# Kernel tuning notes

Measured on AMD Instinct MI355X. Metric: run time of the kernel, lower is better.

Reference implementation:

```python
import jax, jax.numpy as jnp
import numpy as np

B, T, EMB_D, HEAD = 8, 2048, 1024, 128


def setup_inputs() -> dict:
    key = jax.random.key(0)
    ks = jax.random.split(key, 7)
    s = 1.0 / np.sqrt(EMB_D)
    return {
        "inputs": jax.random.normal(ks[0], (B, T, EMB_D), dtype=jnp.float32),
        "Wk": jax.random.uniform(ks[1], (EMB_D, HEAD), jnp.float32, -s, s),
        "bk": jax.random.uniform(ks[2], (HEAD,), jnp.float32, -s, s),
        "Wq": jax.random.uniform(ks[3], (EMB_D, HEAD), jnp.float32, -s, s),
        "bq": jax.random.uniform(ks[4], (HEAD,), jnp.float32, -s, s),
        "Wv": jax.random.uniform(ks[5], (EMB_D, HEAD), jnp.float32, -s, s),
        "bv": jax.random.uniform(ks[6], (HEAD,), jnp.float32, -s, s),
    }


def reference(inputs, Wk, bk, Wq, bq, Wv, bv):
    # inputs: [B, T, C]
    Bq, Tq, _ = inputs.shape
    k = inputs @ Wk + bk  # [B, T, H]
    q = inputs @ Wq + bq
    v = inputs @ Wv + bv
    scale = HEAD ** -0.5
    weights = jnp.einsum("bth,bsh->bts", q, k) * scale  # [B, T, T]
    causal = jnp.tril(jnp.ones((Tq, Tq), dtype=bool))
    weights = jnp.where(causal, weights, -jnp.inf)
    # NOTE: original code applies softmax over dim=1 (the query axis), faithfully reproduced
    weights = jax.nn.softmax(weights, axis=1)
    return jnp.einsum("bts,bsh->bth", weights, v)  # [B, T, H]
```

## Files before the change

### kernel.cpp

```cpp
#include <hip/hip_runtime.h>
#include <hip/hip_bf16.h>

#define T_SEQ 2048
#define NBATCH 8
#define EMB 1024
#define HD 128

typedef _Float16 f16_t;
typedef _Float16 f16x8 __attribute__((ext_vector_type(8)));
typedef _Float16 f16x4 __attribute__((ext_vector_type(4)));
typedef float f32x4 __attribute__((ext_vector_type(4)));


__device__ __forceinline__ void g2l(const f16_t* g, f16_t* l) {
    __builtin_amdgcn_global_load_lds(
        (const __attribute__((address_space(1))) unsigned int*)g,
        (__attribute__((address_space(3))) unsigned int*)l, 16, 0, 0);
}

__global__ __launch_bounds__(256) void prep(
    const float* __restrict__ Wk, const float* __restrict__ bk,
    const float* __restrict__ Wq, const float* __restrict__ bq,
    const float* __restrict__ Wv, const float* __restrict__ bv,
    f16_t* __restrict__ w2, float* __restrict__ biasc,
    float4* __restrict__ out4, float4* __restrict__ colsum4) {
    int bid = blockIdx.x;
    int t = threadIdx.x;
    if (bid < 384) {
        int n = bid;
        const float scale = 0.08838834764831845f;
        const float* W; const float* bias; float sc; int col;
        if (n < 128)      { W = Wq; bias = bq; sc = scale; col = n; }
        else if (n < 256) { W = Wk; bias = bk; sc = 1.0f;  col = n - 128; }
        else              { W = Wv; bias = bv; sc = 1.0f;  col = n - 256; }
        if (t < 128) {
            int k0 = t * 8;
            f16x8 v;
            #pragma unroll
            for (int i = 0; i < 8; ++i) v[i] = (f16_t)(W[(size_t)(k0 + i) * HD + col] * sc);
            *(f16x8*)&w2[(size_t)(n >> 4) * 16384 + (size_t)(k0 >> 3) * 128 + (n & 15) * 8] = v;
        }
        if (t == 0) biasc[n] = bias[col] * sc;
    } else if (bid < 384 + 2048) {
        out4[(size_t)(bid - 384) * 256 + t] = make_float4(0.f, 0.f, 0.f, 0.f);
    } else {
        colsum4[(size_t)(bid - 2432) * 256 + t] = make_float4(0.f, 0.f, 0.f, 0.f);
    }
}

__global__ __launch_bounds__(256) void qkv_gemm(
    const float* __restrict__ X, const f16_t* __restrict__ w2,
    const float* __restrict__ biasc,
    f16_t* __restrict__ q2, f16_t* __restrict__ k2, f16_t* __restrict__ v2) {
    __shared__ f16_t Xs[2][64 * 72];
    __shared__ __align__(16) f16_t Bl[2][8 * 1024];

    int bid = blockIdx.x;
    int r8 = bid & 7, g = bid >> 3;
    int band = (g / 3) * 8 + r8;
    int i = g % 3;
    int m0 = band * 64, n0 = i * 128;
    int tid = threadIdx.x;
    int lane = tid & 63, w = tid >> 6;
    int quad = lane >> 4, l15 = lane & 15;
    int msub = (w & 1) * 32, nsub = (w >> 1) * 64;

    int srow = tid >> 2;
    int scg  = (tid & 3) * 16;

    const float* xrow = X + (size_t)(m0 + srow) * EMB + scg;
    const f16_t* bbase = w2 + (size_t)(n0 >> 4) * 16384;

    f32x4 acc[2][4] = {};
    float4 pf[4];

    auto loadA = [&](int kc) {
        #pragma unroll
        for (int u = 0; u < 4; ++u) pf[u] = *(const float4*)(xrow + kc * 64 + u * 4);
    };
    auto stageB = [&](int kc, int buf) {
        const f16_t* bsrc = bbase + (size_t)kc * 1024;
        #pragma unroll
        for (int ii = 0; ii < 4; ++ii) {
            int D = tid * 16 + ii * 4096;
            g2l(bsrc + (size_t)(D >> 11) * 16384 + ((D & 2047) >> 1),
                &Bl[buf][D >> 1]);
        }
    };
    auto stageA = [&](int buf) {
        union { f16_t h[8]; uint4 u4; } p0, p1;
        p0.h[0] = (f16_t)pf[0].x; p0.h[1] = (f16_t)pf[0].y;
        p0.h[2] = (f16_t)pf[0].z; p0.h[3] = (f16_t)pf[0].w;
        p0.h[4] = (f16_t)pf[1].x; p0.h[5] = (f16_t)pf[1].y;
        p0.h[6] = (f16_t)pf[1].z; p0.h[7] = (f16_t)pf[1].w;
        p1.h[0] = (f16_t)pf[2].x; p1.h[1] = (f16_t)pf[2].y;
        p1.h[2] = (f16_t)pf[2].z; p1.h[3] = (f16_t)pf[2].w;
        p1.h[4] = (f16_t)pf[3].x; p1.h[5] = (f16_t)pf[3].y;
        p1.h[6] = (f16_t)pf[3].z; p1.h[7] = (f16_t)pf[3].w;
        *(uint4*)&Xs[buf][srow * 72 + scg] = p0.u4;
        *(uint4*)&Xs[buf][srow * 72 + scg + 8] = p1.u4;
    };
    auto compute = [&](int buf) {
        #pragma unroll
        for (int ks = 0; ks < 2; ++ks) {
            f16x8 afr0 = *(const f16x8*)&Xs[buf][(msub + l15) * 72 + ks * 32 + quad * 8];
            f16x8 afr1 = *(const f16x8*)&Xs[buf][(msub + 16 + l15) * 72 + ks * 32 + quad * 8];
            #pragma unroll
            for (int nf = 0; nf < 4; ++nf) {
                int ntl = (nsub >> 4) + nf;
                f16x8 bfr = *(const f16x8*)&Bl[buf][ntl * 1024 + (ks * 4 + quad) * 128 + l15 * 8];
                acc[0][nf] = __builtin_amdgcn_mfma_f32_16x16x32_f16(afr0, bfr, acc[0][nf], 0, 0, 0);
                acc[1][nf] = __builtin_amdgcn_mfma_f32_16x16x32_f16(afr1, bfr, acc[1][nf], 0, 0, 0);
            }
        }
    };

    loadA(0);
    stageB(0, 0);
    stageA(0);
    __syncthreads();

    for (int kc = 0; kc < 16; ++kc) {
        int cur = kc & 1, nxt = cur ^ 1;
        if (kc + 1 < 16) {
            loadA(kc + 1);
            stageB(kc + 1, nxt);
        }
        compute(cur);
        if (kc + 1 < 16) stageA(nxt);
        __syncthreads();
    }

    #pragma unroll
    for (int nf = 0; nf < 4; ++nf) {
        int ng = n0 + nsub + nf * 16 + l15;
        float bval = biasc[ng];
        #pragma unroll
        for (int mf = 0; mf < 2; ++mf) {
            int rowg = m0 + msub + mf * 16 + quad * 4;
            f32x4 a = acc[mf][nf];
            if (ng < 256) {
                f16_t* dst = (ng < 128) ? q2 : k2;
                int c = ng & 127;
                #pragma unroll
                for (int r = 0; r < 4; ++r) {
                    int row = rowg + r;
                    dst[(size_t)(row >> 4) * 2048 + (c >> 3) * 128 + (row & 15) * 8 + (c & 7)]
                        = (f16_t)(a[r] + bval);
                }
            } else {
                int h = ng - 256;
                f16x4 hv;
                #pragma unroll
                for (int r = 0; r < 4; ++r) hv[r] = (f16_t)(a[r] + bval);
                *(f16x4*)&v2[(size_t)(rowg >> 3) * 1024 + h * 8 + (rowg & 7)] = hv;
            }
        }
    }
}

__global__ __launch_bounds__(256, 4) void col_stats(
    const f16_t* __restrict__ q2, const f16_t* __restrict__ k2,
    float* __restrict__ colsum) {
    __shared__ __align__(16) f16_t Ql[4 * 2048];

    int bid = blockIdx.x;
    int b = bid & 7;
    int item = 143 - (bid >> 3);
    int cg = 0, slab = 0, cum = 0;
    for (int c = 0; c < 32; ++c) {
        int n = (32 - c + 3) >> 2;
        if (item < cum + n) { cg = c; slab = item - cum; break; }
        cum += n;
    }
    int tc0 = cg + slab * 4, tc1 = min(tc0 + 4, 32);

    int tid = threadIdx.x, lane = tid & 63, w = tid >> 6;
    int quad = lane >> 4, l15 = lane & 15;
    int brow = b * 128;
    size_t base = (size_t)b * T_SEQ;

    f16x8 bfrs[4][4];
    #pragma unroll
    for (int st = 0; st < 4; ++st) {
        const f16_t* kt = k2 + (size_t)(brow + cg * 4 + st) * 2048 + l15 * 8;
        #pragma unroll
        for (int kf = 0; kf < 4; ++kf)
            bfrs[st][kf] = *(const f16x8*)(kt + (kf * 4 + quad) * 128);
    }

    float lacc[4] = {0.f, 0.f, 0.f, 0.f};

    for (int tc = tc0; tc < tc1; ++tc) {
        int tb = tc * 64;
        __syncthreads();
        const f16_t* qsrc = q2 + (size_t)(brow + tc * 4) * 2048;
        #pragma unroll
        for (int i = 0; i < 4; ++i)
            g2l(qsrc + i * 2048 + tid * 8, Ql + i * 2048 + tid * 8);
        __syncthreads();

        f16x8 afr[4];
        #pragma unroll
        for (int kf = 0; kf < 4; ++kf)
            afr[kf] = *(const f16x8*)&Ql[w * 2048 + (kf * 4 + quad) * 128 + l15 * 8];
        #pragma unroll
        for (int st = 0; st < 4; ++st) {
            f32x4 s = {};
            #pragma unroll
            for (int kf = 0; kf < 4; ++kf)
                s = __builtin_amdgcn_mfma_f32_16x16x32_f16(afr[kf], bfrs[st][kf], s, 0, 0, 0);
            int scol = cg * 64 + st * 16 + l15;
            #pragma unroll
            for (int r = 0; r < 4; ++r) {
                int t = tb + w * 16 + quad * 4 + r;
                if (t >= scol) lacc[st] += __expf(s[r]);
            }
        }
    }

    #pragma unroll
    for (int st = 0; st < 4; ++st) {
        float v = lacc[st];
        v += __shfl_xor(v, 16, 64);
        v += __shfl_xor(v, 32, 64);
        if (quad == 0) atomicAdd(&colsum[base + cg * 64 + st * 16 + l15], v);
    }
}

__global__ __launch_bounds__(256, 4) void attn_out(
    const f16_t* __restrict__ q2, const f16_t* __restrict__ k2,
    const f16_t* __restrict__ v2, const float* __restrict__ colsum,
    float* __restrict__ out) {
    __shared__ __align__(16) f16_t Kl[4 * 2048];
    __shared__ __align__(16) f16_t Vl[8 * 1024];
    __shared__ __align__(16) f16_t Pl[32 * 72];

    int bid = blockIdx.x;
    int b = bid & 7;
    int item = 159 - (bid >> 3);
    int g = 0, slab = 0, cum = 0;
    for (int gg = 0; gg < 64; ++gg) {
        int n = (((gg >> 1) + 1) + 7) >> 3;
        if (item < cum + n) { g = gg; slab = item - cum; break; }
        cum += n;
    }
    int nch = (g >> 1) + 1;
    int c0 = slab * 8, c1 = min(c0 + 8, nch);
    int trow = g * 32;

    int tid = threadIdx.x, lane = tid & 63, w = tid >> 6;
    int quad = lane >> 4, l15 = lane & 15;
    int brow = b * 128;
    size_t base = (size_t)b * T_SEQ;

    f16x8 qfr[2][4];
    #pragma unroll
    for (int tt = 0; tt < 2; ++tt) {
        const f16_t* qt = q2 + (size_t)(brow + 2 * g + tt) * 2048 + l15 * 8;
        #pragma unroll
        for (int kf = 0; kf < 4; ++kf)
            qfr[tt][kf] = *(const f16x8*)(qt + (kf * 4 + quad) * 128);
    }

    f32x4 o[2][2] = {};

    for (int c = c0; c < c1; ++c) {
        int sb = c * 64;
        __syncthreads();
        const f16_t* ksrc = k2 + (size_t)(brow + (sb >> 4)) * 2048;
        const f16_t* vsrc = v2 + (((size_t)base + sb) >> 3) * 1024;
        #pragma unroll
        for (int i = 0; i < 4; ++i) {
            g2l(ksrc + i * 2048 + tid * 8, Kl + i * 2048 + tid * 8);
            g2l(vsrc + i * 2048 + tid * 8, Vl + i * 2048 + tid * 8);
        }
        __syncthreads();

        float iv = 1.0f / colsum[base + sb + w * 16 + l15];
        int scol = sb + w * 16 + l15;
        f16x8 bfr[4];
        #pragma unroll
        for (int kf = 0; kf < 4; ++kf)
            bfr[kf] = *(const f16x8*)&Kl[w * 2048 + (kf * 4 + quad) * 128 + l15 * 8];
        #pragma unroll
        for (int tt = 0; tt < 2; ++tt) {
            f32x4 s = {};
            #pragma unroll
            for (int kf = 0; kf < 4; ++kf)
                s = __builtin_amdgcn_mfma_f32_16x16x32_f16(qfr[tt][kf], bfr[kf], s, 0, 0, 0);
            #pragma unroll
            for (int r = 0; r < 4; ++r) {
                int t = trow + tt * 16 + quad * 4 + r;
                float pv = (t >= scol) ? __expf(s[r]) * iv : 0.f;
                Pl[(tt * 16 + quad * 4 + r) * 72 + w * 16 + l15] = (f16_t)pv;
            }
        }
        __syncthreads();

        #pragma unroll
        for (int kf2 = 0; kf2 < 2; ++kf2) {
            f16x8 pa0 = *(const f16x8*)&Pl[(l15) * 72 + kf2 * 32 + quad * 8];
            f16x8 pa1 = *(const f16x8*)&Pl[(16 + l15) * 72 + kf2 * 32 + quad * 8];
            #pragma unroll
            for (int hh = 0; hh < 2; ++hh) {
                f16x8 vfr = *(const f16x8*)&Vl[(kf2 * 4 + quad) * 1024 + (w * 32 + hh * 16 + l15) * 8];
                o[0][hh] = __builtin_amdgcn_mfma_f32_16x16x32_f16(pa0, vfr, o[0][hh], 0, 0, 0);
                o[1][hh] = __builtin_amdgcn_mfma_f32_16x16x32_f16(pa1, vfr, o[1][hh], 0, 0, 0);
            }
        }
    }

    #pragma unroll
    for (int tt = 0; tt < 2; ++tt)
        #pragma unroll
        for (int hh = 0; hh < 2; ++hh)
            #pragma unroll
            for (int r = 0; r < 4; ++r)
                atomicAdd(&out[(base + trow + tt * 16 + quad * 4 + r) * HD + w * 32 + hh * 16 + l15],
                          o[tt][hh][r]);
}

extern "C" void kernel_launch(void* const* d_in, const int* in_sizes, int n_in,
                              void* d_out, int out_size, void* d_ws, size_t ws_size,
                              hipStream_t stream) {
    const float* X  = (const float*)d_in[0];
    const float* Wk = (const float*)d_in[1];
    const float* bk = (const float*)d_in[2];
    const float* Wq = (const float*)d_in[3];
    const float* bq = (const float*)d_in[4];
    const float* Wv = (const float*)d_in[5];
    const float* bv = (const float*)d_in[6];
    float* out = (float*)d_out;

    char* ws = (char*)d_ws;
    const size_t W2_B    = 24 * 16384 * 2;
    const size_t BIAS_B  = 2048;
    const size_t QKV_B   = (size_t)NBATCH * T_SEQ * HD * 2;
    f16_t* w2     = (f16_t*)ws;
    float* biasc  = (float*)(ws + W2_B);
    f16_t* q2     = (f16_t*)(ws + W2_B + BIAS_B);
    f16_t* k2     = (f16_t*)(ws + W2_B + BIAS_B + QKV_B);
    f16_t* v2     = (f16_t*)(ws + W2_B + BIAS_B + 2 * QKV_B);
    float* colsum = (float*)(ws + W2_B + BIAS_B + 3 * QKV_B);

    prep<<<dim3(2448), dim3(256), 0, stream>>>(Wk, bk, Wq, bq, Wv, bv, w2, biasc,
                                               (float4*)out, (float4*)colsum);
    qkv_gemm<<<dim3(768), dim3(256), 0, stream>>>(X, w2, biasc, q2, k2, v2);
    col_stats<<<dim3(1152), dim3(256), 0, stream>>>(q2, k2, colsum);
    attn_out<<<dim3(1280), dim3(256), 0, stream>>>(q2, k2, v2, colsum, out);
}
```

Measured before the change: 174.4 us.

## Load MFMA operands directly from global memory instead of staging through LDS

Across three kernels, operands that were staged in shared memory are now loaded straight from global memory into registers in MFMA fragment layout. In the QKV GEMM the X tile is converted to fp16 in registers rather than written to LDS. In col_stats the Q chunk is loaded per wave. In attn_out the K and V chunks are loaded per wave, with one barrier kept per iteration to guard the P buffer and occupancy lowered to 3 blocks. This removes LDS traffic and barriers but makes more strided global loads rely on L2/L1, and adds register pressure.

```diff
diff --git a/kernel.cpp b/kernel.cpp
--- a/kernel.cpp
+++ b/kernel.cpp
@@ -52,7 +52,6 @@
     const float* __restrict__ X, const f16_t* __restrict__ w2,
     const float* __restrict__ biasc,
     f16_t* __restrict__ q2, f16_t* __restrict__ k2, f16_t* __restrict__ v2) {
-    __shared__ f16_t Xs[2][64 * 72];
     __shared__ __align__(16) f16_t Bl[2][8 * 1024];
 
     int bid = blockIdx.x;
@@ -65,18 +64,33 @@
     int quad = lane >> 4, l15 = lane & 15;
     int msub = (w & 1) * 32, nsub = (w >> 1) * 64;
 
-    int srow = tid >> 2;
-    int scg  = (tid & 3) * 16;
-
-    const float* xrow = X + (size_t)(m0 + srow) * EMB + scg;
+    const float* abase = X + (size_t)(m0 + msub + l15) * EMB + quad * 8;
     const f16_t* bbase = w2 + (size_t)(n0 >> 4) * 16384;
 
     f32x4 acc[2][4] = {};
-    float4 pf[4];
-
-    auto loadA = [&](int kc) {
-        #pragma unroll
-        for (int u = 0; u < 4; ++u) pf[u] = *(const float4*)(xrow + kc * 64 + u * 4);
+    float4 araw[4][2];
+    f16x8 af[4];
+
+    auto loadAraw = [&](int kc) {
+        #pragma unroll
+        for (int mf = 0; mf < 2; ++mf)
+            #pragma unroll
+            for (int ks = 0; ks < 2; ++ks) {
+                const float* p = abase + (size_t)mf * (16 * EMB) + kc * 64 + ks * 32;
+                araw[mf * 2 + ks][0] = *(const float4*)p;
+                araw[mf * 2 + ks][1] = *(const float4*)(p + 4);
+            }
+    };
+    auto cvtA = [&]() {
+        #pragma unroll
+        for (int q = 0; q < 4; ++q) {
+            f16x8 v;
+            v[0] = (f16_t)araw[q][0].x; v[1] = (f16_t)araw[q][0].y;
+            v[2] = (f16_t)araw[q][0].z; v[3] = (f16_t)araw[q][0].w;
+            v[4] = (f16_t)araw[q][1].x; v[5] = (f16_t)araw[q][1].y;
+            v[6] = (f16_t)araw[q][1].z; v[7] = (f16_t)araw[q][1].w;
+            af[q] = v;
+        }
     };
     auto stageB = [&](int kc, int buf) {
         const f16_t* bsrc = bbase + (size_t)kc * 1024;
@@ -87,47 +101,31 @@
                 &Bl[buf][D >> 1]);
         }
     };
-    auto stageA = [&](int buf) {
-        union { f16_t h[8]; uint4 u4; } p0, p1;
-        p0.h[0] = (f16_t)pf[0].x; p0.h[1] = (f16_t)pf[0].y;
-        p0.h[2] = (f16_t)pf[0].z; p0.h[3] = (f16_t)pf[0].w;
-        p0.h[4] = (f16_t)pf[1].x; p0.h[5] = (f16_t)pf[1].y;
-        p0.h[6] = (f16_t)pf[1].z; p0.h[7] = (f16_t)pf[1].w;
-        p1.h[0] = (f16_t)pf[2].x; p1.h[1] = (f16_t)pf[2].y;
-        p1.h[2] = (f16_t)pf[2].z; p1.h[3] = (f16_t)pf[2].w;
-        p1.h[4] = (f16_t)pf[3].x; p1.h[5] = (f16_t)pf[3].y;
-        p1.h[6] = (f16_t)pf[3].z; p1.h[7] = (f16_t)pf[3].w;
-        *(uint4*)&Xs[buf][srow * 72 + scg] = p0.u4;
-        *(uint4*)&Xs[buf][srow * 72 + scg + 8] = p1.u4;
-    };
     auto compute = [&](int buf) {
         #pragma unroll
-        for (int ks = 0; ks < 2; ++ks) {
-            f16x8 afr0 = *(const f16x8*)&Xs[buf][(msub + l15) * 72 + ks * 32 + quad * 8];
-            f16x8 afr1 = *(const f16x8*)&Xs[buf][(msub + 16 + l15) * 72 + ks * 32 + quad * 8];
+        for (int ks = 0; ks < 2; ++ks)
             #pragma unroll
             for (int nf = 0; nf < 4; ++nf) {
                 int ntl = (nsub >> 4) + nf;
                 f16x8 bfr = *(const f16x8*)&Bl[buf][ntl * 1024 + (ks * 4 + quad) * 128 + l15 * 8];
-                acc[0][nf] = __builtin_amdgcn_mfma_f32_16x16x32_f16(afr0, bfr, acc[0][nf], 0, 0, 0);
-                acc[1][nf] = __builtin_amdgcn_mfma_f32_16x16x32_f16(afr1, bfr, acc[1][nf], 0, 0, 0);
-            }
-        }
+                acc[0][nf] = __builtin_amdgcn_mfma_f32_16x16x32_f16(af[ks], bfr, acc[0][nf], 0, 0, 0);
+                acc[1][nf] = __builtin_amdgcn_mfma_f32_16x16x32_f16(af[2 + ks], bfr, acc[1][nf], 0, 0, 0);
+            }
     };
 
-    loadA(0);
+    loadAraw(0);
     stageB(0, 0);
-    stageA(0);
+    cvtA();
     __syncthreads();
 
     for (int kc = 0; kc < 16; ++kc) {
-        int cur = kc & 1, nxt = cur ^ 1;
+        int cur = kc & 1;
         if (kc + 1 < 16) {
-            loadA(kc + 1);
-            stageB(kc + 1, nxt);
+            loadAraw(kc + 1);
+            stageB(kc + 1, cur ^ 1);
         }
         compute(cur);
-        if (kc + 1 < 16) stageA(nxt);
+        if (kc + 1 < 16) cvtA();
         __syncthreads();
     }
 
@@ -162,8 +160,6 @@
 __global__ __launch_bounds__(256, 4) void col_stats(
     const f16_t* __restrict__ q2, const f16_t* __restrict__ k2,
     float* __restrict__ colsum) {
-    __shared__ __align__(16) f16_t Ql[4 * 2048];
-
     int bid = blockIdx.x;
     int b = bid & 7;
     int item = 143 - (bid >> 3);
@@ -193,17 +189,11 @@
 
     for (int tc = tc0; tc < tc1; ++tc) {
         int tb = tc * 64;
-        __syncthreads();
-        const f16_t* qsrc = q2 + (size_t)(brow + tc * 4) * 2048;
-        #pragma unroll
-        for (int i = 0; i < 4; ++i)
-            g2l(qsrc + i * 2048 + tid * 8, Ql + i * 2048 + tid * 8);
-        __syncthreads();
-
         f16x8 afr[4];
+        const f16_t* qt = q2 + (size_t)(brow + tc * 4 + w) * 2048 + l15 * 8;
         #pragma unroll
         for (int kf = 0; kf < 4; ++kf)
-            afr[kf] = *(const f16x8*)&Ql[w * 2048 + (kf * 4 + quad) * 128 + l15 * 8];
+            afr[kf] = *(const f16x8*)(qt + (kf * 4 + quad) * 128);
         #pragma unroll
         for (int st = 0; st < 4; ++st) {
             f32x4 s = {};
@@ -228,12 +218,10 @@
     }
 }
 
-__global__ __launch_bounds__(256, 4) void attn_out(
+__global__ __launch_bounds__(256, 3) void attn_out(
     const f16_t* __restrict__ q2, const f16_t* __restrict__ k2,
     const f16_t* __restrict__ v2, const float* __restrict__ colsum,
     float* __restrict__ out) {
-    __shared__ __align__(16) f16_t Kl[4 * 2048];
-    __shared__ __align__(16) f16_t Vl[8 * 1024];
     __shared__ __align__(16) f16_t Pl[32 * 72];
 
     int bid = blockIdx.x;
@@ -267,22 +255,21 @@
 
     for (int c = c0; c < c1; ++c) {
         int sb = c * 64;
-        __syncthreads();
-        const f16_t* ksrc = k2 + (size_t)(brow + (sb >> 4)) * 2048;
-        const f16_t* vsrc = v2 + (((size_t)base + sb) >> 3) * 1024;
-        #pragma unroll
-        for (int i = 0; i < 4; ++i) {
-            g2l(ksrc + i * 2048 + tid * 8, Kl + i * 2048 + tid * 8);
-            g2l(vsrc + i * 2048 + tid * 8, Vl + i * 2048 + tid * 8);
-        }
-        __syncthreads();
-
+        f16x8 bfr[4];
+        const f16_t* kt = k2 + (size_t)(brow + (sb >> 4) + w) * 2048 + l15 * 8;
+        #pragma unroll
+        for (int kf = 0; kf < 4; ++kf)
+            bfr[kf] = *(const f16x8*)(kt + (kf * 4 + quad) * 128);
+        f16x8 vfr[2][2];
+        const f16_t* vt = v2 + ((size_t)(base + sb) >> 3) * 1024;
+        #pragma unroll
+        for (int kf2 = 0; kf2 < 2; ++kf2)
+            #pragma unroll
+            for (int hh = 0; hh < 2; ++hh)
+                vfr[kf2][hh] = *(const f16x8*)&vt[(kf2 * 4 + quad) * 1024 +
+                                                  (w * 32 + hh * 16 + l15) * 8];
         float iv = 1.0f / colsum[base + sb + w * 16 + l15];
         int scol = sb + w * 16 + l15;
-        f16x8 bfr[4];
-        #pragma unroll
-        for (int kf = 0; kf < 4; ++kf)
-            bfr[kf] = *(const f16x8*)&Kl[w * 2048 + (kf * 4 + quad) * 128 + l15 * 8];
         #pragma unroll
         for (int tt = 0; tt < 2; ++tt) {
             f32x4 s = {};
@@ -304,11 +291,11 @@
             f16x8 pa1 = *(const f16x8*)&Pl[(16 + l15) * 72 + kf2 * 32 + quad * 8];
             #pragma unroll
             for (int hh = 0; hh < 2; ++hh) {
-                f16x8 vfr = *(const f16x8*)&Vl[(kf2 * 4 + quad) * 1024 + (w * 32 + hh * 16 + l15) * 8];
-                o[0][hh] = __builtin_amdgcn_mfma_f32_16x16x32_f16(pa0, vfr, o[0][hh], 0, 0, 0);
-                o[1][hh] = __builtin_amdgcn_mfma_f32_16x16x32_f16(pa1, vfr, o[1][hh], 0, 0, 0);
-            }
-        }
+                o[0][hh] = __builtin_amdgcn_mfma_f32_16x16x32_f16(pa0, vfr[kf2][hh], o[0][hh], 0, 0, 0);
+                o[1][hh] = __builtin_amdgcn_mfma_f32_16x16x32_f16(pa1, vfr[kf2][hh], o[1][hh], 0, 0, 0);
+            }
+        }
+        __syncthreads();
     }
 
     #pragma unroll
```

Result: slower. 192.2 us (+10.2%).

## Drop LDS staging; split key chunks across waves with register-resident P

Applied to the files above, without the earlier changes.

col_stats now reads Q fragments straight from global memory instead of staging them through LDS, which removes two barriers per tile. attn_out is restructured so each wave owns a separate 16-key slice rather than the 64-key chunk being shared across waves. It computes S transposed so the exp'd P tile stays in registers and feeds a 16x16x16 MFMA against V loaded directly from global, with each wave accumulating all 128 head columns. Per-wave partials are reduced serially in LDS before atomically adding to the output. This removes the K/V/P LDS round-trips and per-chunk barriers, but raises register pressure (launch bound lowered to 3 waves) and loses cross-wave reuse of global K/V loads.

```diff
diff --git a/kernel.cpp b/kernel.cpp
--- a/kernel.cpp
+++ b/kernel.cpp
@@ -162,8 +162,6 @@
 __global__ __launch_bounds__(256, 4) void col_stats(
     const f16_t* __restrict__ q2, const f16_t* __restrict__ k2,
     float* __restrict__ colsum) {
-    __shared__ __align__(16) f16_t Ql[4 * 2048];
-
     int bid = blockIdx.x;
     int b = bid & 7;
     int item = 143 - (bid >> 3);
@@ -193,17 +191,11 @@
 
     for (int tc = tc0; tc < tc1; ++tc) {
         int tb = tc * 64;
-        __syncthreads();
-        const f16_t* qsrc = q2 + (size_t)(brow + tc * 4) * 2048;
-        #pragma unroll
-        for (int i = 0; i < 4; ++i)
-            g2l(qsrc + i * 2048 + tid * 8, Ql + i * 2048 + tid * 8);
-        __syncthreads();
-
         f16x8 afr[4];
+        const f16_t* qt = q2 + (size_t)(brow + tc * 4 + w) * 2048 + l15 * 8;
         #pragma unroll
         for (int kf = 0; kf < 4; ++kf)
-            afr[kf] = *(const f16x8*)&Ql[w * 2048 + (kf * 4 + quad) * 128 + l15 * 8];
+            afr[kf] = *(const f16x8*)(qt + (kf * 4 + quad) * 128);
         #pragma unroll
         for (int st = 0; st < 4; ++st) {
             f32x4 s = {};
@@ -228,13 +220,11 @@
     }
 }
 
-__global__ __launch_bounds__(256, 4) void attn_out(
+__global__ __launch_bounds__(256, 3) void attn_out(
     const f16_t* __restrict__ q2, const f16_t* __restrict__ k2,
     const f16_t* __restrict__ v2, const float* __restrict__ colsum,
     float* __restrict__ out) {
-    __shared__ __align__(16) f16_t Kl[4 * 2048];
-    __shared__ __align__(16) f16_t Vl[8 * 1024];
-    __shared__ __align__(16) f16_t Pl[32 * 72];
+    __shared__ float Or[32 * 128];
 
     int bid = blockIdx.x;
     int b = bid & 7;
@@ -263,62 +253,69 @@
             qfr[tt][kf] = *(const f16x8*)(qt + (kf * 4 + quad) * 128);
     }
 
-    f32x4 o[2][2] = {};
-
-    for (int c = c0; c < c1; ++c) {
-        int sb = c * 64;
+    f32x4 o[2][8] = {};
+
+    for (int j = c0 * 4 + w; j < c1 * 4; j += 4) {
+        int s0 = j * 16;
+        f16x8 kfr[4];
+        const f16_t* kt = k2 + (size_t)(brow + j) * 2048 + l15 * 8;
+        #pragma unroll
+        for (int kf = 0; kf < 4; ++kf)
+            kfr[kf] = *(const f16x8*)(kt + (kf * 4 + quad) * 128);
+
+        f32x4 st[2] = {};
+        #pragma unroll
+        for (int tt = 0; tt < 2; ++tt)
+            #pragma unroll
+            for (int kf = 0; kf < 4; ++kf)
+                st[tt] = __builtin_amdgcn_mfma_f32_16x16x32_f16(
+                    kfr[kf], qfr[tt][kf], st[tt], 0, 0, 0);
+
+        float4 cs = *(const float4*)&colsum[base + s0 + quad * 4];
+        float iv0 = 1.0f / cs.x, iv1 = 1.0f / cs.y,
+              iv2 = 1.0f / cs.z, iv3 = 1.0f / cs.w;
+        int sg = s0 + quad * 4;
+        f16x4 p[2];
+        #pragma unroll
+        for (int tt = 0; tt < 2; ++tt) {
+            int t = trow + tt * 16 + l15;
+            float p0 = (t >= sg + 0) ? __expf(st[tt][0]) * iv0 : 0.f;
+            float p1 = (t >= sg + 1) ? __expf(st[tt][1]) * iv1 : 0.f;
+            float p2 = (t >= sg + 2) ? __expf(st[tt][2]) * iv2 : 0.f;
+            float p3 = (t >= sg + 3) ? __expf(st[tt][3]) * iv3 : 0.f;
+            p[tt][0] = (f16_t)p0; p[tt][1] = (f16_t)p1;
+            p[tt][2] = (f16_t)p2; p[tt][3] = (f16_t)p3;
+        }
+
+        const f16_t* vt = v2 + ((size_t)(base + s0) >> 3) * 1024 +
+                          (quad >> 1) * 1024 + (quad & 1) * 4;
+        #pragma unroll
+        for (int h8 = 0; h8 < 8; ++h8) {
+            f16x4 vf = *(const f16x4*)&vt[(h8 * 16 + l15) * 8];
+            o[0][h8] = __builtin_amdgcn_mfma_f32_16x16x16f16(p[0], vf, o[0][h8], 0, 0, 0);
+            o[1][h8] = __builtin_amdgcn_mfma_f32_16x16x16f16(p[1], vf, o[1][h8], 0, 0, 0);
+        }
+    }
+
+    #pragma unroll 1
+    for (int wp = 0; wp < 4; ++wp) {
+        if (w == wp) {
+            #pragma unroll
+            for (int tt = 0; tt < 2; ++tt)
+                #pragma unroll
+                for (int h8 = 0; h8 < 8; ++h8)
+                    #pragma unroll
+                    for (int r = 0; r < 4; ++r) {
+                        int idx = (tt * 16 + quad * 4 + r) * 128 + h8 * 16 + l15;
+                        if (wp == 0) Or[idx] = o[tt][h8][r];
+                        else         Or[idx] += o[tt][h8][r];
+                    }
+        }
         __syncthreads();
-        const f16_t* ksrc = k2 + (size_t)(brow + (sb >> 4)) * 2048;
-        const f16_t* vsrc = v2 + (((size_t)base + sb) >> 3) * 1024;
-        #pragma unroll
-        for (int i = 0; i < 4; ++i) {
-            g2l(ksrc + i * 2048 + tid * 8, Kl + i * 2048 + tid * 8);
-            g2l(vsrc + i * 2048 + tid * 8, Vl + i * 2048 + tid * 8);
-        }
-        __syncthreads();
-
-        float iv = 1.0f / colsum[base + sb + w * 16 + l15];
-        int scol = sb + w * 16 + l15;
-        f16x8 bfr[4];
-        #pragma unroll
-        for (int kf = 0; kf < 4; ++kf)
-            bfr[kf] = *(const f16x8*)&Kl[w * 2048 + (kf * 4 + quad) * 128 + l15 * 8];
-        #pragma unroll
-        for (int tt = 0; tt < 2; ++tt) {
-            f32x4 s = {};
-            #pragma unroll
-            for (int kf = 0; kf < 4; ++kf)
-                s = __builtin_amdgcn_mfma_f32_16x16x32_f16(qfr[tt][kf], bfr[kf], s, 0, 0, 0);
-            #pragma unroll
-            for (int r = 0; r < 4; ++r) {
-                int t = trow + tt * 16 + quad * 4 + r;
-                float pv = (t >= scol) ? __expf(s[r]) * iv : 0.f;
-                Pl[(tt * 16 + quad * 4 + r) * 72 + w * 16 + l15] = (f16_t)pv;
-            }
-        }
-        __syncthreads();
-
-        #pragma unroll
-        for (int kf2 = 0; kf2 < 2; ++kf2) {
-            f16x8 pa0 = *(const f16x8*)&Pl[(l15) * 72 + kf2 * 32 + quad * 8];
-            f16x8 pa1 = *(const f16x8*)&Pl[(16 + l15) * 72 + kf2 * 32 + quad * 8];
-            #pragma unroll
-            for (int hh = 0; hh < 2; ++hh) {
-                f16x8 vfr = *(const f16x8*)&Vl[(kf2 * 4 + quad) * 1024 + (w * 32 + hh * 16 + l15) * 8];
-                o[0][hh] = __builtin_amdgcn_mfma_f32_16x16x32_f16(pa0, vfr, o[0][hh], 0, 0, 0);
-                o[1][hh] = __builtin_amdgcn_mfma_f32_16x16x32_f16(pa1, vfr, o[1][hh], 0, 0, 0);
-            }
-        }
-    }
-
-    #pragma unroll
-    for (int tt = 0; tt < 2; ++tt)
-        #pragma unroll
-        for (int hh = 0; hh < 2; ++hh)
-            #pragma unroll
-            for (int r = 0; r < 4; ++r)
-                atomicAdd(&out[(base + trow + tt * 16 + quad * 4 + r) * HD + w * 32 + hh * 16 + l15],
-                          o[tt][hh][r]);
+    }
+    float* ob = out + (base + trow) * HD;
+    for (int idx = tid; idx < 32 * 128; idx += 256)
+        atomicAdd(&ob[((idx >> 7)) * HD + (idx & 127)], Or[idx]);
 }
 
 extern "C" void kernel_launch(void* const* d_in, const int* in_sizes, int n_in,
```

New measurement: 198.4 us. 13.8% more time.

## Read GEMM weights and Q fragments directly from global memory, halve GEMM tile width

Applied to the files above, without the earlier changes.

In qkv_gemm, the LDS staging of the weight tile is dropped and B fragments are loaded straight from global memory (relying on cache hits). The N tile shrinks from 128 to 64, doubling the grid to 1536 blocks, with a launch bound targeting 6 blocks per CU. In col_stats, the Q tile is read directly into registers from global memory instead of through LDS, which removes two barriers per iteration. The goal is less LDS use and fewer syncs for higher occupancy, at the cost of uncoalesced global loads and more global traffic for X, since each block now covers less of N.

```diff
diff --git a/kernel.cpp b/kernel.cpp
--- a/kernel.cpp
+++ b/kernel.cpp
@@ -48,44 +48,34 @@
     }
 }
 
-__global__ __launch_bounds__(256) void qkv_gemm(
+__global__ __launch_bounds__(256, 6) void qkv_gemm(
     const float* __restrict__ X, const f16_t* __restrict__ w2,
     const float* __restrict__ biasc,
     f16_t* __restrict__ q2, f16_t* __restrict__ k2, f16_t* __restrict__ v2) {
     __shared__ f16_t Xs[2][64 * 72];
-    __shared__ __align__(16) f16_t Bl[2][8 * 1024];
 
     int bid = blockIdx.x;
     int r8 = bid & 7, g = bid >> 3;
-    int band = (g / 3) * 8 + r8;
-    int i = g % 3;
-    int m0 = band * 64, n0 = i * 128;
+    int band = (g / 6) * 8 + r8;
+    int n0 = (g % 6) * 64;
+    int m0 = band * 64;
     int tid = threadIdx.x;
     int lane = tid & 63, w = tid >> 6;
     int quad = lane >> 4, l15 = lane & 15;
-    int msub = (w & 1) * 32, nsub = (w >> 1) * 64;
+    int msub = (w & 1) * 32, nsub = (w >> 1) * 32;
 
     int srow = tid >> 2;
     int scg  = (tid & 3) * 16;
 
     const float* xrow = X + (size_t)(m0 + srow) * EMB + scg;
-    const f16_t* bbase = w2 + (size_t)(n0 >> 4) * 16384;
-
-    f32x4 acc[2][4] = {};
+    int ntbase = (n0 >> 4) + (nsub >> 4);
+
+    f32x4 acc[2][2] = {};
     float4 pf[4];
 
     auto loadA = [&](int kc) {
         #pragma unroll
         for (int u = 0; u < 4; ++u) pf[u] = *(const float4*)(xrow + kc * 64 + u * 4);
-    };
-    auto stageB = [&](int kc, int buf) {
-        const f16_t* bsrc = bbase + (size_t)kc * 1024;
-        #pragma unroll
-        for (int ii = 0; ii < 4; ++ii) {
-            int D = tid * 16 + ii * 4096;
-            g2l(bsrc + (size_t)(D >> 11) * 16384 + ((D & 2047) >> 1),
-                &Bl[buf][D >> 1]);
-        }
     };
     auto stageA = [&](int buf) {
         union { f16_t h[8]; uint4 u4; } p0, p1;
@@ -100,15 +90,15 @@
         *(uint4*)&Xs[buf][srow * 72 + scg] = p0.u4;
         *(uint4*)&Xs[buf][srow * 72 + scg + 8] = p1.u4;
     };
-    auto compute = [&](int buf) {
+    auto compute = [&](int kc, int buf) {
         #pragma unroll
         for (int ks = 0; ks < 2; ++ks) {
             f16x8 afr0 = *(const f16x8*)&Xs[buf][(msub + l15) * 72 + ks * 32 + quad * 8];
             f16x8 afr1 = *(const f16x8*)&Xs[buf][(msub + 16 + l15) * 72 + ks * 32 + quad * 8];
             #pragma unroll
-            for (int nf = 0; nf < 4; ++nf) {
-                int ntl = (nsub >> 4) + nf;
-                f16x8 bfr = *(const f16x8*)&Bl[buf][ntl * 1024 + (ks * 4 + quad) * 128 + l15 * 8];
+            for (int nf = 0; nf < 2; ++nf) {
+                f16x8 bfr = *(const f16x8*)&w2[(size_t)(ntbase + nf) * 16384 +
+                    (size_t)(kc * 8 + ks * 4 + quad) * 128 + l15 * 8];
                 acc[0][nf] = __builtin_amdgcn_mfma_f32_16x16x32_f16(afr0, bfr, acc[0][nf], 0, 0, 0);
                 acc[1][nf] = __builtin_amdgcn_mfma_f32_16x16x32_f16(afr1, bfr, acc[1][nf], 0, 0, 0);
             }
@@ -116,23 +106,19 @@
     };
 
     loadA(0);
-    stageB(0, 0);
     stageA(0);
     __syncthreads();
 
     for (int kc = 0; kc < 16; ++kc) {
-        int cur = kc & 1, nxt = cur ^ 1;
-        if (kc + 1 < 16) {
-            loadA(kc + 1);
-            stageB(kc + 1, nxt);
-        }
-        compute(cur);
-        if (kc + 1 < 16) stageA(nxt);
+        int cur = kc & 1;
+        if (kc + 1 < 16) loadA(kc + 1);
+        compute(kc, cur);
+        if (kc + 1 < 16) stageA(cur ^ 1);
         __syncthreads();
     }
 
     #pragma unroll
-    for (int nf = 0; nf < 4; ++nf) {
+    for (int nf = 0; nf < 2; ++nf) {
         int ng = n0 + nsub + nf * 16 + l15;
         float bval = biasc[ng];
         #pragma unroll
@@ -162,8 +148,6 @@
 __global__ __launch_bounds__(256, 4) void col_stats(
     const f16_t* __restrict__ q2, const f16_t* __restrict__ k2,
     float* __restrict__ colsum) {
-    __shared__ __align__(16) f16_t Ql[4 * 2048];
-
     int bid = blockIdx.x;
     int b = bid & 7;
     int item = 143 - (bid >> 3);
@@ -193,17 +177,11 @@
 
     for (int tc = tc0; tc < tc1; ++tc) {
         int tb = tc * 64;
-        __syncthreads();
-        const f16_t* qsrc = q2 + (size_t)(brow + tc * 4) * 2048;
-        #pragma unroll
-        for (int i = 0; i < 4; ++i)
-            g2l(qsrc + i * 2048 + tid * 8, Ql + i * 2048 + tid * 8);
-        __syncthreads();
-
         f16x8 afr[4];
+        const f16_t* qt = q2 + (size_t)(brow + tc * 4 + w) * 2048 + l15 * 8;
         #pragma unroll
         for (int kf = 0; kf < 4; ++kf)
-            afr[kf] = *(const f16x8*)&Ql[w * 2048 + (kf * 4 + quad) * 128 + l15 * 8];
+            afr[kf] = *(const f16x8*)(qt + (kf * 4 + quad) * 128);
         #pragma unroll
         for (int st = 0; st < 4; ++st) {
             f32x4 s = {};
@@ -346,7 +324,7 @@
 
     prep<<<dim3(2448), dim3(256), 0, stream>>>(Wk, bk, Wq, bq, Wv, bv, w2, biasc,
                                                (float4*)out, (float4*)colsum);
-    qkv_gemm<<<dim3(768), dim3(256), 0, stream>>>(X, w2, biasc, q2, k2, v2);
+    qkv_gemm<<<dim3(1536), dim3(256), 0, stream>>>(X, w2, biasc, q2, k2, v2);
     col_stats<<<dim3(1152), dim3(256), 0, stream>>>(q2, k2, colsum);
     attn_out<<<dim3(1280), dim3(256), 0, stream>>>(q2, k2, v2, colsum, out);
 }
```

Result: slower. 189.1 us (+8.4%).
